# Optimization experiments

Measured on AMD Instinct MI355X. Metric: run time of the kernel, lower is better.

Reference implementation:

```python
import jax, jax.numpy as jnp
import numpy as np

DEPTH = 4
HEADS = 8
DIM = 512
MLP = 2048
EPS = 1e-5


def layernorm(x, w, b):
    m = x.mean(-1, keepdims=True)
    v = x.var(-1, keepdims=True)
    return (x - m) * jax.lax.rsqrt(v + EPS) * w + b


def setup_inputs() -> dict:
    key = jax.random.key(0)
    ks = jax.random.split(key, 6)
    s = 0.02
    x = jax.random.normal(ks[0], (4, 2048, DIM), dtype=jnp.float32)
    return {
        "x": x,
        "ln1_w": jnp.ones((DEPTH, DIM), jnp.float32),
        "ln1_b": jnp.zeros((DEPTH, DIM), jnp.float32),
        "qkv_w": jax.random.normal(ks[1], (DEPTH, 3 * DIM, DIM), jnp.float32) * s,
        "proj_w": jax.random.normal(ks[2], (DEPTH, DIM, DIM), jnp.float32) * s,
        "proj_b": jnp.zeros((DEPTH, DIM), jnp.float32),
        "ln2_w": jnp.ones((DEPTH, DIM), jnp.float32),
        "ln2_b": jnp.zeros((DEPTH, DIM), jnp.float32),
        "fc1_w": jax.random.normal(ks[3], (DEPTH, MLP, DIM), jnp.float32) * s,
        "fc1_b": jnp.zeros((DEPTH, MLP), jnp.float32),
        "fc2_w": jax.random.normal(ks[4], (DEPTH, DIM, MLP), jnp.float32) * s,
        "fc2_b": jnp.zeros((DEPTH, DIM), jnp.float32),
    }


def reference(x, ln1_w, ln1_b, qkv_w, proj_w, proj_b, ln2_w, ln2_b, fc1_w, fc1_b, fc2_w, fc2_b):
    B, N, C = x.shape
    Dh = C // HEADS
    scale = Dh ** (-0.5)
    for i in range(DEPTH):
        # PreNorm attention block
        h = layernorm(x, ln1_w[i], ln1_b[i])
        qkv = (h @ qkv_w[i].T).reshape(B, N, 3, HEADS, Dh).transpose(2, 0, 3, 1, 4)
        q, k, v = qkv[0], qkv[1], qkv[2]          # [B,H,N,Dh]
        attn = jax.nn.softmax(jnp.einsum('bhnd,bhmd->bhnm', q, k) * scale, axis=-1)
        o = jnp.einsum('bhnm,bhmd->bhnd', attn, v).transpose(0, 2, 1, 3).reshape(B, N, C)
        x = o @ proj_w[i].T + proj_b[i] + x
        # PreNorm FFN block (exact erf GELU, matching torch nn.GELU default)
        h = layernorm(x, ln2_w[i], ln2_b[i])
        h = jax.nn.gelu(h @ fc1_w[i].T + fc1_b[i], approximate=False)
        x = h @ fc2_w[i].T + fc2_b[i] + x
    return x
```

## Files before the change

### kernel.cpp

```cpp
#include <hip/hip_runtime.h>
#include <hip/hip_bf16.h>
#include <math.h>

#define NB 4
#define HEADS 8
#define DIM 512
#define MLP 2048
#define NT 2048
#define DH 64
#define M_TOK (NB*NT)

typedef __bf16 bf16;
typedef __bf16 bf16x4 __attribute__((ext_vector_type(4)));
typedef __bf16 bf16x8 __attribute__((ext_vector_type(8)));
typedef float f32x4 __attribute__((ext_vector_type(4)));

__device__ __forceinline__ void gl_lds16(const void* g, void* l) {
    __builtin_amdgcn_global_load_lds((const __attribute__((address_space(1))) unsigned int*)g,
                                     (__attribute__((address_space(3))) unsigned int*)l, 16, 0, 0);
}

__global__ void cvt_bf16_kernel(const float* __restrict__ src, bf16* __restrict__ dst, int n) {
    int i = (blockIdx.x * 256 + threadIdx.x) * 4;
    if (i < n) {
        float4 v = *(const float4*)(src + i);
        bf16x4 o;
        o[0] = (bf16)v.x; o[1] = (bf16)v.y; o[2] = (bf16)v.z; o[3] = (bf16)v.w;
        *(bf16x4*)(dst + i) = o;
    }
}

__global__ void ln_kernel(const float* __restrict__ X, const float* __restrict__ gam,
                          const float* __restrict__ bet, bf16* __restrict__ out) {
    int w = threadIdx.x >> 6, l = threadIdx.x & 63;
    long row = (long)blockIdx.x * 4 + w;
    const float* xp = X + row * DIM + l * 8;
    float4 a = *(const float4*)xp;
    float4 b = *(const float4*)(xp + 4);
    float s1 = a.x + a.y + a.z + a.w + b.x + b.y + b.z + b.w;
    float s2 = a.x*a.x + a.y*a.y + a.z*a.z + a.w*a.w + b.x*b.x + b.y*b.y + b.z*b.z + b.w*b.w;
#pragma unroll
    for (int off = 32; off; off >>= 1) { s1 += __shfl_xor(s1, off); s2 += __shfl_xor(s2, off); }
    float mean = s1 * (1.f / 512.f);
    float var  = s2 * (1.f / 512.f) - mean * mean;
    float rstd = rsqrtf(var + 1e-5f);
    float4 g0 = *(const float4*)(gam + l * 8), g1 = *(const float4*)(gam + l * 8 + 4);
    float4 b0 = *(const float4*)(bet + l * 8), b1 = *(const float4*)(bet + l * 8 + 4);
    bf16x8 o;
    o[0] = (bf16)((a.x - mean) * rstd * g0.x + b0.x);
    o[1] = (bf16)((a.y - mean) * rstd * g0.y + b0.y);
    o[2] = (bf16)((a.z - mean) * rstd * g0.z + b0.z);
    o[3] = (bf16)((a.w - mean) * rstd * g0.w + b0.w);
    o[4] = (bf16)((b.x - mean) * rstd * g1.x + b1.x);
    o[5] = (bf16)((b.y - mean) * rstd * g1.y + b1.y);
    o[6] = (bf16)((b.z - mean) * rstd * g1.z + b1.z);
    o[7] = (bf16)((b.w - mean) * rstd * g1.w + b1.w);
    *(bf16x8*)(out + row * DIM + l * 8) = o;
}

template<int EPI>
__global__ void gemm_bt(const bf16* __restrict__ A, const bf16* __restrict__ W,
                        const float* __restrict__ bias, const float* resid,
                        void* outp, int M, int N, int K) {
    __shared__ bf16 As[128 * 64];
    __shared__ bf16 Bs[128 * 64];
    int t = threadIdx.x, w = t >> 6, l = t & 63;
    int wr = w >> 1, wc = w & 1, g = l >> 4, c = l & 15;
    long arow0 = (long)blockIdx.y * 128, bcol0 = (long)blockIdx.x * 128;
    f32x4 acc[4][4] = {};
    int lrow = l >> 3, lcol = (l & 7) * 8;
    const bf16* Ab = A + (arow0 + lrow) * (long)K + lcol;
    const bf16* Wb = W + (bcol0 + lrow) * (long)K + lcol;
    for (int k0 = 0; k0 < K; k0 += 64) {
#pragma unroll
        for (int q = 0; q < 4; ++q) {
            int ci = w * 4 + q;
            gl_lds16(Ab + (long)ci * 8 * K + k0, &As[ci * 512]);
            gl_lds16(Wb + (long)ci * 8 * K + k0, &Bs[ci * 512]);
        }
        __syncthreads();
#pragma unroll
        for (int kk = 0; kk < 2; ++kk) {
            bf16x8 af[4], bfr[4];
#pragma unroll
            for (int m = 0; m < 4; ++m) af[m]  = *(const bf16x8*)&As[(wr * 64 + m * 16 + c) * 64 + kk * 32 + g * 8];
#pragma unroll
            for (int n = 0; n < 4; ++n) bfr[n] = *(const bf16x8*)&Bs[(wc * 64 + n * 16 + c) * 64 + kk * 32 + g * 8];
#pragma unroll
            for (int m = 0; m < 4; ++m)
#pragma unroll
                for (int n = 0; n < 4; ++n)
                    acc[m][n] = __builtin_amdgcn_mfma_f32_16x16x32_bf16(af[m], bfr[n], acc[m][n], 0, 0, 0);
        }
        __syncthreads();
    }
#pragma unroll
    for (int m = 0; m < 4; ++m)
#pragma unroll
        for (int n = 0; n < 4; ++n) {
            long row = arow0 + wr * 64 + m * 16 + g * 4;
            long col = bcol0 + wc * 64 + n * 16 + c;
#pragma unroll
            for (int r = 0; r < 4; ++r) {
                float v = acc[m][n][r];
                long rr = row + r;
                if constexpr (EPI == 0) {
                    int o = (int)col;
                    int s = o >> 9, hh = (o >> 6) & 7, d = o & 63;
                    int b = (int)(rr >> 11), nn = (int)(rr & 2047);
                    ((bf16*)outp)[(((long)(s * NB + b) * HEADS + hh) * NT + nn) * DH + d] = (bf16)v;
                } else if constexpr (EPI == 1) {
                    ((float*)outp)[rr * N + col] = v + bias[col] + resid[rr * N + col];
                } else {
                    float u = v + bias[col];
                    float ge = 0.5f * u * (1.f + erff(u * 0.70710678118654752f));
                    ((bf16*)outp)[rr * N + col] = (bf16)ge;
                }
            }
        }
}

__global__ void attn_kernel(const bf16* __restrict__ qkv, bf16* __restrict__ O) {
    __shared__ bf16 Ks[64 * 64];
    __shared__ bf16 Vt[64 * 64];
    int t = threadIdx.x, w = t >> 6, l = t & 63;
    int g = l >> 4, c = l & 15;
    int qt = blockIdx.x, bh = blockIdx.y;
    long headoff = (long)bh * (NT * DH);
    const bf16* Qb = qkv + headoff;
    const bf16* Kb = qkv + (long)(NB * HEADS) * (NT * DH) + headoff;
    const bf16* Vb = qkv + (long)2 * (NB * HEADS) * (NT * DH) + headoff;
    int q0 = qt * 64 + w * 16;
    bf16x8 qf[2];
    qf[0] = *(const bf16x8*)(Qb + (long)(q0 + c) * DH + g * 8);
    qf[1] = *(const bf16x8*)(Qb + (long)(q0 + c) * DH + 32 + g * 8);
    f32x4 oacc[4] = {};
    float mrun = -__builtin_inff(), lrun = 0.f;
    const float scale = 0.125f;
    int skey = t >> 3, sdh = (t & 7) * 8;
    int vdh = t & 63, vkg = t >> 6;

    for (int kt = 0; kt < NT / 64; ++kt) {
        int key0 = kt * 64;
#pragma unroll
        for (int p = 0; p < 2; ++p) {
            int key = p * 32 + skey;
            bf16x8 kv = *(const bf16x8*)(Kb + (long)(key0 + key) * DH + sdh);
            *(bf16x8*)&Ks[(key * 64 + sdh) ^ ((key & 7) << 3)] = kv;
        }
        {
            const bf16* vp = Vb + (long)(key0 + vkg * 16) * DH + vdh;
            alignas(16) bf16 tmp[16];
#pragma unroll
            for (int i = 0; i < 16; ++i) tmp[i] = vp[(long)i * DH];
            *(bf16x8*)&Vt[(vdh * 64 + vkg * 16) ^ ((vdh & 7) << 3)]     = *(bf16x8*)&tmp[0];
            *(bf16x8*)&Vt[(vdh * 64 + vkg * 16 + 8) ^ ((vdh & 7) << 3)] = *(bf16x8*)&tmp[8];
        }
        __syncthreads();
        f32x4 st[4] = {};
#pragma unroll
        for (int kk = 0; kk < 2; ++kk)
#pragma unroll
            for (int kc = 0; kc < 4; ++kc) {
                int key = kc * 16 + c;
                bf16x8 kf = *(const bf16x8*)&Ks[(key * 64 + kk * 32 + g * 8) ^ ((key & 7) << 3)];
                st[kc] = __builtin_amdgcn_mfma_f32_16x16x32_bf16(kf, qf[kk], st[kc], 0, 0, 0);
            }
        float pv[4][4];
        float mt = -__builtin_inff();
#pragma unroll
        for (int kc = 0; kc < 4; ++kc)
#pragma unroll
            for (int r = 0; r < 4; ++r) { float sv = st[kc][r] * scale; pv[kc][r] = sv; mt = fmaxf(mt, sv); }
        mt = fmaxf(mt, __shfl_xor(mt, 16));
        mt = fmaxf(mt, __shfl_xor(mt, 32));
        float mnew = fmaxf(mrun, mt);
        float fr = __expf(mrun - mnew);
        float ssum = 0.f;
#pragma unroll
        for (int kc = 0; kc < 4; ++kc)
#pragma unroll
            for (int r = 0; r < 4; ++r) { float p = __expf(pv[kc][r] - mnew); pv[kc][r] = p; ssum += p; }
        ssum += __shfl_xor(ssum, 16);
        ssum += __shfl_xor(ssum, 32);
        lrun = lrun * fr + ssum;
        mrun = mnew;
#pragma unroll
        for (int dc = 0; dc < 4; ++dc) oacc[dc] *= fr;
        bf16x8 pf[2];
#pragma unroll
        for (int ks = 0; ks < 2; ++ks)
#pragma unroll
            for (int j = 0; j < 8; ++j) pf[ks][j] = (bf16)pv[2 * ks + (j >> 2)][j & 3];
#pragma unroll
        for (int dc = 0; dc < 4; ++dc) {
            int dh = dc * 16 + c;
            int hwb = dh * 64, sw = (dh & 7) << 3;
#pragma unroll
            for (int ks = 0; ks < 2; ++ks) {
                bf16x4 v0 = *(const bf16x4*)&Vt[(hwb + ks * 32 + g * 4) ^ sw];
                bf16x4 v1 = *(const bf16x4*)&Vt[(hwb + ks * 32 + 16 + g * 4) ^ sw];
                bf16x8 vf = __builtin_shufflevector(v0, v1, 0, 1, 2, 3, 4, 5, 6, 7);
                oacc[dc] = __builtin_amdgcn_mfma_f32_16x16x32_bf16(vf, pf[ks], oacc[dc], 0, 0, 0);
            }
        }
        __syncthreads();
    }
    float inv = 1.f / lrun;
    bf16* ol = &Ks[w * 1024];
#pragma unroll
    for (int dc = 0; dc < 4; ++dc)
#pragma unroll
        for (int r = 0; r < 4; ++r)
            ol[c * 64 + dc * 16 + g * 4 + r] = (bf16)(oacc[dc][r] * inv);
    int qq = l >> 2, dh0 = (l & 3) * 16;
    int b = bh >> 3, hh = bh & 7;
    bf16x8 r0 = *(const bf16x8*)&ol[qq * 64 + dh0];
    bf16x8 r1 = *(const bf16x8*)&ol[qq * 64 + dh0 + 8];
    long tok = (long)b * NT + q0 + qq;
    *(bf16x8*)(O + tok * DIM + hh * 64 + dh0) = r0;
    *(bf16x8*)(O + tok * DIM + hh * 64 + dh0 + 8) = r1;
}

extern "C" void kernel_launch(void* const* d_in, const int* in_sizes, int n_in,
                              void* d_out, int out_size, void* d_ws, size_t ws_size,
                              hipStream_t stream) {
    const float* x      = (const float*)d_in[0];
    const float* ln1_w  = (const float*)d_in[1];
    const float* ln1_b  = (const float*)d_in[2];
    const float* qkv_w  = (const float*)d_in[3];
    const float* proj_w = (const float*)d_in[4];
    const float* proj_b = (const float*)d_in[5];
    const float* ln2_w  = (const float*)d_in[6];
    const float* ln2_b  = (const float*)d_in[7];
    const float* fc1_w  = (const float*)d_in[8];
    const float* fc1_b  = (const float*)d_in[9];
    const float* fc2_w  = (const float*)d_in[10];
    const float* fc2_b  = (const float*)d_in[11];
    float* X = (float*)d_out;

    char* ws = (char*)d_ws;
    bf16* h_bf   = (bf16*)(ws);
    bf16* scr_bf = (bf16*)(ws + (size_t)(8  << 20));
    bf16* o_bf   = (bf16*)(ws + (size_t)(40 << 20));
    bf16* w_qkv  = (bf16*)(ws + (size_t)(48 << 20));
    bf16* w_proj = w_qkv  + (size_t)4 * 1536 * 512;
    bf16* w_fc1  = w_proj + (size_t)4 * 512 * 512;
    bf16* w_fc2  = w_fc1  + (size_t)4 * 2048 * 512;

    {
        int n;
        n = 4 * 1536 * 512; cvt_bf16_kernel<<<n / 1024, 256, 0, stream>>>(qkv_w,  w_qkv,  n);
        n = 4 * 512 * 512;  cvt_bf16_kernel<<<n / 1024, 256, 0, stream>>>(proj_w, w_proj, n);
        n = 4 * 2048 * 512; cvt_bf16_kernel<<<n / 1024, 256, 0, stream>>>(fc1_w,  w_fc1,  n);
        n = 4 * 512 * 2048; cvt_bf16_kernel<<<n / 1024, 256, 0, stream>>>(fc2_w,  w_fc2,  n);
    }
    hipMemcpyAsync(X, x, (size_t)M_TOK * DIM * sizeof(float), hipMemcpyDeviceToDevice, stream);

    for (int i = 0; i < 4; ++i) {
        ln_kernel<<<M_TOK / 4, 256, 0, stream>>>(X, ln1_w + i * 512, ln1_b + i * 512, h_bf);
        gemm_bt<0><<<dim3(12, 64), 256, 0, stream>>>(h_bf, w_qkv + (size_t)i * 1536 * 512,
                                                     nullptr, nullptr, scr_bf, M_TOK, 1536, 512);
        attn_kernel<<<dim3(32, 32), 256, 0, stream>>>(scr_bf, o_bf);
        gemm_bt<1><<<dim3(4, 64), 256, 0, stream>>>(o_bf, w_proj + (size_t)i * 512 * 512,
                                                    proj_b + i * 512, X, X, M_TOK, 512, 512);
        ln_kernel<<<M_TOK / 4, 256, 0, stream>>>(X, ln2_w + i * 512, ln2_b + i * 512, h_bf);
        gemm_bt<2><<<dim3(16, 64), 256, 0, stream>>>(h_bf, w_fc1 + (size_t)i * 2048 * 512,
                                                     fc1_b + i * 2048, nullptr, scr_bf, M_TOK, 2048, 512);
        gemm_bt<1><<<dim3(4, 64), 256, 0, stream>>>(scr_bf, w_fc2 + (size_t)i * 512 * 2048,
                                                    fc2_b + i * 512, X, X, M_TOK, 512, 2048);
    }
}
```

Baseline: 863.0 us.

## Add pipelined 256x256 double-buffered GEMM for QKV and FC1 projections

Adds a new 512-thread GEMM kernel with 256x256 tiles and double-buffered LDS. Global-to-LDS loads are interleaved with MFMA quarters under explicit vmcnt waits and barriers. It also uses XOR-swizzled LDS addressing, XCD-aware block remapping and s_setprio around the MFMA bursts. It is used for the QKV and FC1 projections, which are meant to gain from more data reuse and from overlapping loads with compute. The old kernel is kept only for the residual-add projections. Risks are larger register and LDS use, which could limit occupancy, and fewer blocks per grid (192 and 256).

Result: no change. 857.8 us (-0.6%).

```diff
diff --git a/kernel.cpp b/kernel.cpp
--- a/kernel.cpp
+++ b/kernel.cpp
@@ -19,6 +19,10 @@
     __builtin_amdgcn_global_load_lds((const __attribute__((address_space(1))) unsigned int*)g,
                                      (__attribute__((address_space(3))) unsigned int*)l, 16, 0, 0);
 }
+
+#define BARRIER() do { __builtin_amdgcn_s_barrier(); asm volatile("" ::: "memory"); } while(0)
+#define WAIT_VM4() asm volatile("s_waitcnt vmcnt(4)" ::: "memory")
+#define WAIT_VM0() asm volatile("s_waitcnt vmcnt(0)" ::: "memory")
 
 __global__ void cvt_bf16_kernel(const float* __restrict__ src, bf16* __restrict__ dst, int n) {
     int i = (blockIdx.x * 256 + threadIdx.x) * 4;
@@ -58,10 +62,144 @@
     *(bf16x8*)(out + row * DIM + l * 8) = o;
 }
 
+#define KDIM 512
+
+#define LOADA(AF, B_, MQ) do { \
+  _Pragma("unroll") for (int mi_ = 0; mi_ < 4; ++mi_) \
+  _Pragma("unroll") for (int kk_ = 0; kk_ < 2; ++kk_) { \
+    int row_ = wr * 128 + ((MQ) * 4 + mi_) * 16 + c; \
+    AF[mi_][kk_] = *(const bf16x8*)&Abuf[B_][row_ * 64 + (((kk_ * 64 + g * 16) ^ sw) >> 1)]; \
+  } } while (0)
+
+#define LOADB(BF, B_, NQ) do { \
+  _Pragma("unroll") for (int ni_ = 0; ni_ < 2; ++ni_) \
+  _Pragma("unroll") for (int kk_ = 0; kk_ < 2; ++kk_) { \
+    int row_ = wc * 64 + ((NQ) * 2 + ni_) * 16 + c; \
+    BF[ni_][kk_] = *(const bf16x8*)&Bbuf[B_][row_ * 64 + (((kk_ * 64 + g * 16) ^ sw) >> 1)]; \
+  } } while (0)
+
+#define MFMA16(AF, BF, MQ, NQ) do { \
+  __builtin_amdgcn_s_setprio(1); \
+  _Pragma("unroll") for (int mi_ = 0; mi_ < 4; ++mi_) \
+  _Pragma("unroll") for (int ni_ = 0; ni_ < 2; ++ni_) \
+  _Pragma("unroll") for (int kk_ = 0; kk_ < 2; ++kk_) \
+    acc[(MQ)*4+mi_][(NQ)*2+ni_] = __builtin_amdgcn_mfma_f32_16x16x32_bf16( \
+        AF[mi_][kk_], BF[ni_][kk_], acc[(MQ)*4+mi_][(NQ)*2+ni_], 0, 0, 0); \
+  __builtin_amdgcn_s_setprio(0); \
+} while (0)
+
+#define STAGE_A(J_, MQ) do { int j_ = (J_); if (j_ < nkt) { \
+  bf16* db_ = Abuf[j_ & 1]; const bf16* sb_ = Aptr + (size_t)j_ * 64 + coloff; \
+  _Pragma("unroll") for (int q_ = 0; q_ < 2; ++q_) { \
+    int rpl_ = (MQ) * 64 + q_ * 128 + r0; \
+    int rwb_ = (MQ) * 64 + q_ * 128 + (w << 3); \
+    gl_lds16(sb_ + (size_t)(arow0 + rpl_) * KDIM, db_ + rwb_ * 64); \
+  } } } while (0)
+
+#define STAGE_B(J_, NQ) do { int j_ = (J_); if (j_ < nkt) { \
+  bf16* db_ = Bbuf[j_ & 1]; const bf16* sb_ = Wptr + (size_t)j_ * 64 + coloff; \
+  _Pragma("unroll") for (int q_ = 0; q_ < 2; ++q_) { \
+    int rpl_ = q_ * 128 + ((r0 >> 5) << 6) + (NQ) * 32 + (r0 & 31); \
+    int rwb_ = q_ * 128 + (((w << 3) >> 5) << 6) + (NQ) * 32 + ((w << 3) & 31); \
+    gl_lds16(sb_ + (size_t)(bcol0 + rpl_) * KDIM, db_ + rwb_ * 64); \
+  } } } while (0)
+
 template<int EPI>
+__global__ __launch_bounds__(512, 2) void gemm256(const bf16* __restrict__ Aptr,
+                                                  const bf16* __restrict__ Wptr,
+                                                  const float* __restrict__ bias,
+                                                  void* outp, int M, int N) {
+    __shared__ bf16 Abuf[2][256 * 64];
+    __shared__ bf16 Bbuf[2][256 * 64];
+    const int t = threadIdx.x, w = t >> 6, l = t & 63;
+    const int wr = w >> 2, wc = w & 3, g = l >> 4, c = l & 15;
+    const int sw = (c & 7) << 4;
+    const int r0 = (w << 3) + (l >> 3);
+    const int coloff = ((l & 7) ^ (l >> 3)) << 3;
+
+    int nwg = gridDim.x;
+    int bid = blockIdx.x;
+    int q8 = nwg >> 3, r8 = nwg & 7;
+    int xcd = bid & 7, rank = bid >> 3;
+    int swz = (xcd < r8) ? xcd * (q8 + 1) + rank : r8 * (q8 + 1) + (xcd - r8) * q8 + rank;
+    int tiles_n = N >> 8;
+    long arow0 = (long)(swz / tiles_n) * 256;
+    long bcol0 = (long)(swz % tiles_n) * 256;
+
+    const int nkt = KDIM / 64;
+    const int niter = nkt / 2;
+    f32x4 acc[8][4] = {};
+    bf16x8 af[4][2], bn0[2][2], bn1[2][2];
+
+    STAGE_A(0, 0); STAGE_B(0, 0); STAGE_A(0, 1); STAGE_B(0, 1);
+    STAGE_A(1, 0); STAGE_B(1, 0);
+
+#pragma unroll 1
+    for (int tt = 0; tt < niter; ++tt) {
+        const int J0 = 2 * tt, J1 = 2 * tt + 1;
+        const bool last = (tt == niter - 1);
+        WAIT_VM4(); BARRIER();
+        LOADA(af, 0, 0); LOADB(bn0, 0, 0);
+        STAGE_A(J0 + 1, 1);
+        MFMA16(af, bn0, 0, 0);
+        BARRIER();
+        LOADB(bn1, 0, 1);
+        STAGE_B(J0 + 1, 1);
+        MFMA16(af, bn1, 0, 1);
+        BARRIER();
+        LOADA(af, 0, 1);
+        STAGE_A(J0 + 2, 0);
+        MFMA16(af, bn0, 1, 0);
+        BARRIER();
+        STAGE_B(J0 + 2, 0);
+        MFMA16(af, bn1, 1, 1);
+        BARRIER();
+        if (last) { WAIT_VM0(); } else { WAIT_VM4(); }
+        BARRIER();
+        LOADA(af, 1, 0); LOADB(bn0, 1, 0);
+        STAGE_A(J1 + 1, 1);
+        MFMA16(af, bn0, 0, 0);
+        BARRIER();
+        LOADB(bn1, 1, 1);
+        STAGE_B(J1 + 1, 1);
+        MFMA16(af, bn1, 0, 1);
+        BARRIER();
+        LOADA(af, 1, 1);
+        STAGE_A(J1 + 2, 0);
+        MFMA16(af, bn0, 1, 0);
+        BARRIER();
+        STAGE_B(J1 + 2, 0);
+        MFMA16(af, bn1, 1, 1);
+        BARRIER();
+    }
+
+#pragma unroll
+    for (int m = 0; m < 8; ++m)
+#pragma unroll
+        for (int n = 0; n < 4; ++n) {
+            long row = arow0 + wr * 128 + m * 16 + g * 4;
+            long col = bcol0 + wc * 64 + n * 16 + c;
+#pragma unroll
+            for (int r = 0; r < 4; ++r) {
+                float v = acc[m][n][r];
+                long rr = row + r;
+                if constexpr (EPI == 0) {
+                    int o = (int)col;
+                    int s = o >> 9, hh = (o >> 6) & 7, d = o & 63;
+                    int b = (int)(rr >> 11), nn = (int)(rr & 2047);
+                    ((bf16*)outp)[(((long)(s * NB + b) * HEADS + hh) * NT + nn) * DH + d] = (bf16)v;
+                } else {
+                    float u = v + bias[col];
+                    float ge = 0.5f * u * (1.f + erff(u * 0.70710678118654752f));
+                    ((bf16*)outp)[rr * N + col] = (bf16)ge;
+                }
+            }
+        }
+}
+
 __global__ void gemm_bt(const bf16* __restrict__ A, const bf16* __restrict__ W,
                         const float* __restrict__ bias, const float* resid,
-                        void* outp, int M, int N, int K) {
+                        float* outp, int M, int N, int K) {
     __shared__ bf16 As[128 * 64];
     __shared__ bf16 Bs[128 * 64];
     int t = threadIdx.x, w = t >> 6, l = t & 63;
@@ -81,16 +219,16 @@
         __syncthreads();
 #pragma unroll
         for (int kk = 0; kk < 2; ++kk) {
-            bf16x8 af[4], bfr[4];
-#pragma unroll
-            for (int m = 0; m < 4; ++m) af[m]  = *(const bf16x8*)&As[(wr * 64 + m * 16 + c) * 64 + kk * 32 + g * 8];
+            bf16x8 afv[4], bfr[4];
+#pragma unroll
+            for (int m = 0; m < 4; ++m) afv[m] = *(const bf16x8*)&As[(wr * 64 + m * 16 + c) * 64 + kk * 32 + g * 8];
 #pragma unroll
             for (int n = 0; n < 4; ++n) bfr[n] = *(const bf16x8*)&Bs[(wc * 64 + n * 16 + c) * 64 + kk * 32 + g * 8];
 #pragma unroll
             for (int m = 0; m < 4; ++m)
 #pragma unroll
                 for (int n = 0; n < 4; ++n)
-                    acc[m][n] = __builtin_amdgcn_mfma_f32_16x16x32_bf16(af[m], bfr[n], acc[m][n], 0, 0, 0);
+                    acc[m][n] = __builtin_amdgcn_mfma_f32_16x16x32_bf16(afv[m], bfr[n], acc[m][n], 0, 0, 0);
         }
         __syncthreads();
     }
@@ -102,20 +240,8 @@
             long col = bcol0 + wc * 64 + n * 16 + c;
 #pragma unroll
             for (int r = 0; r < 4; ++r) {
-                float v = acc[m][n][r];
                 long rr = row + r;
-                if constexpr (EPI == 0) {
-                    int o = (int)col;
-                    int s = o >> 9, hh = (o >> 6) & 7, d = o & 63;
-                    int b = (int)(rr >> 11), nn = (int)(rr & 2047);
-                    ((bf16*)outp)[(((long)(s * NB + b) * HEADS + hh) * NT + nn) * DH + d] = (bf16)v;
-                } else if constexpr (EPI == 1) {
-                    ((float*)outp)[rr * N + col] = v + bias[col] + resid[rr * N + col];
-                } else {
-                    float u = v + bias[col];
-                    float ge = 0.5f * u * (1.f + erff(u * 0.70710678118654752f));
-                    ((bf16*)outp)[rr * N + col] = (bf16)ge;
-                }
+                outp[rr * N + col] = acc[m][n][r] + bias[col] + resid[rr * N + col];
             }
         }
 }
@@ -195,11 +321,11 @@
 #pragma unroll
         for (int dc = 0; dc < 4; ++dc) {
             int dh = dc * 16 + c;
-            int hwb = dh * 64, sw = (dh & 7) << 3;
+            int hwb = dh * 64, swv = (dh & 7) << 3;
 #pragma unroll
             for (int ks = 0; ks < 2; ++ks) {
-                bf16x4 v0 = *(const bf16x4*)&Vt[(hwb + ks * 32 + g * 4) ^ sw];
-                bf16x4 v1 = *(const bf16x4*)&Vt[(hwb + ks * 32 + 16 + g * 4) ^ sw];
+                bf16x4 v0 = *(const bf16x4*)&Vt[(hwb + ks * 32 + g * 4) ^ swv];
+                bf16x4 v1 = *(const bf16x4*)&Vt[(hwb + ks * 32 + 16 + g * 4) ^ swv];
                 bf16x8 vf = __builtin_shufflevector(v0, v1, 0, 1, 2, 3, 4, 5, 6, 7);
                 oacc[dc] = __builtin_amdgcn_mfma_f32_16x16x32_bf16(vf, pf[ks], oacc[dc], 0, 0, 0);
             }
@@ -259,15 +385,15 @@
 
     for (int i = 0; i < 4; ++i) {
         ln_kernel<<<M_TOK / 4, 256, 0, stream>>>(X, ln1_w + i * 512, ln1_b + i * 512, h_bf);
-        gemm_bt<0><<<dim3(12, 64), 256, 0, stream>>>(h_bf, w_qkv + (size_t)i * 1536 * 512,
-                                                     nullptr, nullptr, scr_bf, M_TOK, 1536, 512);
+        gemm256<0><<<(M_TOK / 256) * (1536 / 256), 512, 0, stream>>>(
+            h_bf, w_qkv + (size_t)i * 1536 * 512, nullptr, scr_bf, M_TOK, 1536);
         attn_kernel<<<dim3(32, 32), 256, 0, stream>>>(scr_bf, o_bf);
-        gemm_bt<1><<<dim3(4, 64), 256, 0, stream>>>(o_bf, w_proj + (size_t)i * 512 * 512,
-                                                    proj_b + i * 512, X, X, M_TOK, 512, 512);
+        gemm_bt<<<dim3(4, 64), 256, 0, stream>>>(o_bf, w_proj + (size_t)i * 512 * 512,
+                                                 proj_b + i * 512, X, X, M_TOK, 512, 512);
         ln_kernel<<<M_TOK / 4, 256, 0, stream>>>(X, ln2_w + i * 512, ln2_b + i * 512, h_bf);
-        gemm_bt<2><<<dim3(16, 64), 256, 0, stream>>>(h_bf, w_fc1 + (size_t)i * 2048 * 512,
-                                                     fc1_b + i * 2048, nullptr, scr_bf, M_TOK, 2048, 512);
-        gemm_bt<1><<<dim3(4, 64), 256, 0, stream>>>(scr_bf, w_fc2 + (size_t)i * 512 * 2048,
-                                                    fc2_b + i * 512, X, X, M_TOK, 512, 2048);
-    }
-}
+        gemm256<2><<<(M_TOK / 256) * (2048 / 256), 512, 0, stream>>>(
+            h_bf, w_fc1 + (size_t)i * 2048 * 512, fc1_b + i * 2048, scr_bf, M_TOK, 2048);
+        gemm_bt<<<dim3(4, 64), 256, 0, stream>>>(scr_bf, w_fc2 + (size_t)i * 512 * 2048,
+                                                 fc2_b + i * 512, X, X, M_TOK, 512, 2048);
+    }
+}
```
